# Kernel tuning notes

Measured on AMD Instinct MI355X. Metric: run time of the kernel, lower is better.

The kernel has to match this reference:

```python
import jax, jax.numpy as jnp
import numpy as np

# Model constants (from init_kwargs, post tensor-parallel split with world_size=8)
N_LOCAL_HEADS = 4      # 32 // 8
N_LOCAL_KV_HEADS = 1   # 8 // 8
N_REP = 4              # local q heads per kv head
HEAD_DIM = 128         # 4096 // 32
ROPE_THETA = 500000.0
EPS = 1e-6
FLOOR_SCALE = 8192.0
ATTN_SCALE = 0.1


def setup_inputs() -> dict:
    key = jax.random.key(0)
    ks = jax.random.split(key, 5)
    B, S, D = 4, 2048, 4096
    x = jax.random.normal(ks[0], (B, S, D), dtype=jnp.float32)
    positions = jnp.arange(S, dtype=jnp.int32)
    w_std = 0.02
    wq = jax.random.normal(ks[1], (D, N_LOCAL_HEADS * HEAD_DIM), dtype=jnp.float32) * w_std
    wk = jax.random.normal(ks[2], (D, N_LOCAL_KV_HEADS * HEAD_DIM), dtype=jnp.float32) * w_std
    wv = jax.random.normal(ks[3], (D, N_LOCAL_KV_HEADS * HEAD_DIM), dtype=jnp.float32) * w_std
    wo = jax.random.normal(ks[4], (N_LOCAL_HEADS * HEAD_DIM, D), dtype=jnp.float32) * w_std
    return {"x": x, "positions": positions, "wq": wq, "wk": wk, "wv": wv, "wo": wo}


def _apply_rope(t, cos, sin):
    # t: [B, S, h, HEAD_DIM]; interleaved complex pairs as in torch view_as_complex
    B, S, h, hd = t.shape
    tr = t.reshape(B, S, h, hd // 2, 2)
    t0, t1 = tr[..., 0], tr[..., 1]
    c = cos[None, :, None, :]  # [1, S, 1, hd//2]
    s = sin[None, :, None, :]
    o0 = t0 * c - t1 * s
    o1 = t0 * s + t1 * c
    return jnp.stack([o0, o1], axis=-1).reshape(B, S, h, hd)


def _rms_norm(t):
    # QK-norm: L2/RMS norm over head_dim, no learnable weight (Llama4 style)
    return t * jax.lax.rsqrt(jnp.mean(t * t, axis=-1, keepdims=True) + EPS)


def reference(x, positions, wq, wk, wv, wo):
    B, S, D = x.shape
    q = (x @ wq).reshape(B, S, N_LOCAL_HEADS, HEAD_DIM)
    k = (x @ wk).reshape(B, S, N_LOCAL_KV_HEADS, HEAD_DIM)
    v = (x @ wv).reshape(B, S, N_LOCAL_KV_HEADS, HEAD_DIM)

    # RoPE angles
    pos_f = positions.astype(jnp.float32)
    inv_freq = 1.0 / (ROPE_THETA ** (jnp.arange(0, HEAD_DIM, 2, dtype=jnp.float32) / HEAD_DIM))
    ang = pos_f[:, None] * inv_freq[None, :]  # [S, HEAD_DIM//2]
    cos, sin = jnp.cos(ang), jnp.sin(ang)

    q = _apply_rope(q, cos, sin)
    k = _apply_rope(k, cos, sin)

    # QK RMSNorm (applied after rope)
    q = _rms_norm(q)
    k = _rms_norm(k)

    # Temperature-tuned query scaling (per absolute position)
    attn_scales = jnp.log(jnp.floor((pos_f + 1.0) / FLOOR_SCALE) + 1.0) * ATTN_SCALE + 1.0
    q = q * attn_scales[None, :, None, None]

    # GQA: repeat kv heads to match local query heads
    k = jnp.repeat(k, N_REP, axis=2)  # [B, S, H, hd]
    v = jnp.repeat(v, N_REP, axis=2)

    scale = 1.0 / jnp.sqrt(jnp.float32(HEAD_DIM))
    scores = jnp.einsum("bqhd,bkhd->bhqk", q, k) * scale  # [B, H, S, S]
    causal = jnp.tril(jnp.ones((S, S), dtype=bool))
    scores = jnp.where(causal[None, None, :, :], scores, jnp.finfo(scores.dtype).min)
    probs = jax.nn.softmax(scores, axis=-1)
    attn = jnp.einsum("bhqk,bkhd->bqhd", probs, v).reshape(B, S, N_LOCAL_HEADS * HEAD_DIM)
    return attn @ wo
```

## Files before the change

kernel.cpp:

```cpp
#include <hip/hip_runtime.h>

typedef unsigned short u16;
typedef unsigned int u32;
typedef __bf16 bf16x8 __attribute__((ext_vector_type(8)));
typedef __bf16 bf16x2 __attribute__((ext_vector_type(2)));
typedef float f32x4 __attribute__((ext_vector_type(4)));

#define S_LEN 2048

__device__ __forceinline__ u16 f2b(float f) {
    union { float f; unsigned u; } a; a.f = f;
    unsigned u = a.u;
    unsigned r = u + 0x7fffu + ((u >> 16) & 1u);
    return (u16)(r >> 16);
}

__device__ __forceinline__ u32 pk2(float a, float b) {
    return (u32)f2b(a) | ((u32)f2b(b) << 16);
}

__device__ __forceinline__ u32 cvt2(float lo, float hi) {
    union { bf16x2 v; u32 u; } c;
    c.v[0] = (__bf16)lo; c.v[1] = (__bf16)hi;
    return c.u;
}

__device__ __forceinline__ void gload16(const void* g, void* l) {
    __builtin_amdgcn_global_load_lds(
        (const __attribute__((address_space(1))) unsigned int*)g,
        (__attribute__((address_space(3))) unsigned int*)l,
        16, 0, 0);
}

__global__ __launch_bounds__(256) void pack_wqkv_kernel(const float* __restrict__ wq,
                                                        const float* __restrict__ wk,
                                                        const float* __restrict__ wv,
                                                        u16* __restrict__ W) {
    __shared__ float t[32][33];
    const int n0 = blockIdx.x * 32, k0 = blockIdx.y * 32;
    const int tid = threadIdx.x;
    const int cc = tid & 31, rr = tid >> 5;
    #pragma unroll
    for (int i = 0; i < 4; ++i) {
        int k = k0 + rr + i * 8, n = n0 + cc;
        float v;
        if (n < 512)      v = wq[(size_t)k * 512 + n];
        else if (n < 640) v = wk[(size_t)k * 128 + (n - 512)];
        else              v = wv[(size_t)k * 128 + (n - 640)];
        t[rr + i * 8][cc] = v;
    }
    __syncthreads();
    #pragma unroll
    for (int i = 0; i < 4; ++i) {
        int nn = rr + i * 8, kk = cc;
        W[(size_t)(n0 + nn) * 4096 + k0 + kk] = f2b(t[kk][nn]);
    }
}

__global__ __launch_bounds__(256) void pack_wo_kernel(const float* __restrict__ wo,
                                                      u16* __restrict__ W) {
    __shared__ float t[32][33];
    const int n0 = blockIdx.x * 32, k0 = blockIdx.y * 32;
    const int tid = threadIdx.x;
    const int cc = tid & 31, rr = tid >> 5;
    #pragma unroll
    for (int i = 0; i < 4; ++i)
        t[rr + i * 8][cc] = wo[(size_t)(k0 + rr + i * 8) * 4096 + n0 + cc];
    __syncthreads();
    #pragma unroll
    for (int i = 0; i < 4; ++i)
        W[(size_t)(n0 + rr + i * 8) * 512 + k0 + cc] = f2b(t[cc][rr + i * 8]);
}

__global__ __launch_bounds__(256) void gemm_cvt(const float* __restrict__ A,
                                                const u16* __restrict__ B,
                                                float* __restrict__ C0,
                                                float* __restrict__ C1,
                                                int N, int K, int kBase) {
    __shared__ __align__(16) u16 sB[3][128 * 32];
    __shared__ __align__(16) u16 sAw[4][64 * 40];
    const int tid = threadIdx.x;
    const int lane = tid & 63, wid = tid >> 6;
    const int wr = wid >> 1, wc = wid & 1;
    const int l15 = lane & 15, g = lane >> 4;
    const int srow = lane >> 2;
    const int swzc = ((lane & 3) * 8) ^ (((lane >> 3) & 3) << 3);
    const int rswz = ((l15 >> 1) & 3) << 3;

    const u32 lid = blockIdx.x + gridDim.x * (blockIdx.y + gridDim.y * blockIdx.z);
    const u32 xcd = lid & 7, slot = lid >> 3;
    const u32 per = gridDim.x * gridDim.z;
    const u32 bml = slot / per;
    const u32 rmd = slot - bml * per;
    const int bn = rmd % gridDim.x;
    const int z  = rmd / gridDim.x;
    const int bm = xcd * (gridDim.y >> 3) + bml;

    float* C = z ? C1 : C0;
    const int k0 = z * kBase;
    const int nt = kBase / 32;

    const int ch0 = wid * 2, ch1 = wid * 2 + 1;
    const int br0 = ch0 * 16 + srow, br1 = ch1 * 16 + srow;

    auto stageB = [&](int buf, int kt) {
        gload16(&B[(size_t)(bn * 128 + br0) * K + kt + swzc], &sB[buf][ch0 * 512]);
        gload16(&B[(size_t)(bn * 128 + br1) * K + kt + swzc], &sB[buf][ch1 * 512]);
    };

    const int alr = lane >> 3, alc = (lane & 7) * 4;
    const float* Abase = A + (size_t)(bm * 128 + wr * 64 + alr) * K + alc;

    float4 raw[8];
    auto issueA = [&](int kt) {
        #pragma unroll
        for (int i = 0; i < 8; ++i)
            raw[i] = *(const float4*)(Abase + (size_t)(8 * i) * K + kt);
    };
    auto writeA = [&]() {
        #pragma unroll
        for (int i = 0; i < 8; ++i) {
            uint2 w;
            w.x = cvt2(raw[i].x, raw[i].y);
            w.y = cvt2(raw[i].z, raw[i].w);
            *(uint2*)&sAw[wid][(8 * i + alr) * 40 + alc] = w;
        }
    };

    f32x4 acc[4][4] = {};

    issueA(k0);
    stageB(0, k0);
    stageB(1, k0 + 32);

    for (int t = 0; t < nt; ++t) {
        if (t + 1 < nt) asm volatile("s_waitcnt vmcnt(2)" ::: "memory");
        else            asm volatile("s_waitcnt vmcnt(0)" ::: "memory");
        __builtin_amdgcn_s_barrier();
        writeA();
        if (t + 1 < nt) issueA(k0 + (t + 1) * 32);
        if (t + 2 < nt) stageB((t + 2) % 3, k0 + (t + 2) * 32);
        __builtin_amdgcn_sched_barrier(0);
        const int cur = t % 3;
        bf16x8 af[4], bfr[4];
        #pragma unroll
        for (int m = 0; m < 4; ++m)
            af[m] = *(const bf16x8*)&sAw[wid][(m * 16 + l15) * 40 + g * 8];
        #pragma unroll
        for (int n = 0; n < 4; ++n)
            bfr[n] = *(const bf16x8*)&sB[cur][(wc * 64 + n * 16 + l15) * 32 + (g * 8 ^ rswz)];
        #pragma unroll
        for (int m = 0; m < 4; ++m)
            #pragma unroll
            for (int n = 0; n < 4; ++n)
                acc[m][n] = __builtin_amdgcn_mfma_f32_16x16x32_bf16(af[m], bfr[n], acc[m][n], 0, 0, 0);
    }

    #pragma unroll
    for (int m = 0; m < 4; ++m) {
        int row = bm * 128 + wr * 64 + m * 16 + g * 4;
        #pragma unroll
        for (int n = 0; n < 4; ++n) {
            int col = bn * 128 + wc * 64 + n * 16 + l15;
            #pragma unroll
            for (int rr = 0; rr < 4; ++rr)
                C[(size_t)(row + rr) * N + col] = acc[m][n][rr];
        }
    }
}

__global__ __launch_bounds__(256) void gemm_pipe(const u16* __restrict__ A,
                                                 const u16* __restrict__ B,
                                                 float* __restrict__ C,
                                                 int N, int K) {
    __shared__ __align__(16) u16 sA[3][128 * 32];
    __shared__ __align__(16) u16 sB[3][128 * 32];
    const int tid = threadIdx.x;
    const int lane = tid & 63, wid = tid >> 6;
    const int wr = wid >> 1, wc = wid & 1;
    const int l15 = lane & 15, g = lane >> 4;
    const int srow = lane >> 2;
    const int swzc = ((lane & 3) * 8) ^ (((lane >> 3) & 3) << 3);
    const int rswz = ((l15 >> 1) & 3) << 3;

    const u32 lid = blockIdx.x + gridDim.x * blockIdx.y;
    const u32 xcd = lid & 7, slot = lid >> 3;
    const u32 per = gridDim.x;
    const u32 bml = slot / per;
    const int bn = slot - bml * per;
    const int bm = xcd * (gridDim.y >> 3) + bml;

    const int nt = K / 32;
    const int ch0 = wid * 2, ch1 = wid * 2 + 1;
    const int r0 = ch0 * 16 + srow, r1 = ch1 * 16 + srow;

    auto stage = [&](int buf, int kt) {
        gload16(&A[(size_t)(bm * 128 + r0) * K + kt + swzc], &sA[buf][ch0 * 512]);
        gload16(&A[(size_t)(bm * 128 + r1) * K + kt + swzc], &sA[buf][ch1 * 512]);
        gload16(&B[(size_t)(bn * 128 + r0) * K + kt + swzc], &sB[buf][ch0 * 512]);
        gload16(&B[(size_t)(bn * 128 + r1) * K + kt + swzc], &sB[buf][ch1 * 512]);
    };

    f32x4 acc[4][4] = {};

    stage(0, 0);
    stage(1, 32);

    for (int t = 0; t < nt; ++t) {
        if (t + 1 < nt) asm volatile("s_waitcnt vmcnt(4)" ::: "memory");
        else            asm volatile("s_waitcnt vmcnt(0)" ::: "memory");
        __builtin_amdgcn_s_barrier();
        __builtin_amdgcn_sched_barrier(0);
        if (t + 2 < nt) stage((t + 2) % 3, (t + 2) * 32);
        const int cur = t % 3;
        bf16x8 af[4], bfr[4];
        #pragma unroll
        for (int m = 0; m < 4; ++m)
            af[m] = *(const bf16x8*)&sA[cur][(wr * 64 + m * 16 + l15) * 32 + (g * 8 ^ rswz)];
        #pragma unroll
        for (int n = 0; n < 4; ++n)
            bfr[n] = *(const bf16x8*)&sB[cur][(wc * 64 + n * 16 + l15) * 32 + (g * 8 ^ rswz)];
        #pragma unroll
        for (int m = 0; m < 4; ++m)
            #pragma unroll
            for (int n = 0; n < 4; ++n)
                acc[m][n] = __builtin_amdgcn_mfma_f32_16x16x32_bf16(af[m], bfr[n], acc[m][n], 0, 0, 0);
    }

    #pragma unroll
    for (int m = 0; m < 4; ++m) {
        int row = bm * 128 + wr * 64 + m * 16 + g * 4;
        #pragma unroll
        for (int n = 0; n < 4; ++n) {
            int col = bn * 128 + wc * 64 + n * 16 + l15;
            #pragma unroll
            for (int rr = 0; rr < 4; ++rr)
                C[(size_t)(row + rr) * N + col] = acc[m][n][rr];
        }
    }
}

__global__ __launch_bounds__(256) void rope_rms_kernel(const float* __restrict__ P0,
                                                       const float* __restrict__ P1,
                                                       const int* __restrict__ positions,
                                                       u16* __restrict__ Qb,
                                                       u16* __restrict__ Kb) {
    const int w = blockIdx.x * 4 + (threadIdx.x >> 6);
    const int lane = threadIdx.x & 63;
    const int row = w / 5, head = w - row * 5;
    const int s = row & (S_LEN - 1);

    float pos = (float)positions[s];
    float ex = (float)(2 * lane) * (1.0f / 128.0f);
    float inv_freq = __expf(-ex * 13.122363377404328f);
    float ang = pos * inv_freq;
    float c, sn;
    __sincosf(ang, &sn, &c);

    size_t off = (size_t)row * 768 + head * 128 + 2 * lane;
    float2 va = *(const float2*)&P0[off];
    float2 vb = *(const float2*)&P1[off];
    float x0 = va.x + vb.x, x1 = va.y + vb.y;
    float o0 = x0 * c - x1 * sn;
    float o1 = x0 * sn + x1 * c;

    float ss = o0 * o0 + o1 * o1;
    #pragma unroll
    for (int m = 1; m < 64; m <<= 1) ss += __shfl_xor(ss, m, 64);
    float rms = rsqrtf(ss * (1.0f / 128.0f) + 1e-6f);

    if (head < 4) {
        float ascale = logf(floorf((pos + 1.0f) * (1.0f / 8192.0f)) + 1.0f) * 0.1f + 1.0f;
        float mult = rms * ascale * 0.12751743f;
        *(u32*)&Qb[(size_t)row * 512 + head * 128 + 2 * lane] = pk2(o0 * mult, o1 * mult);
    } else {
        *(u32*)&Kb[(size_t)row * 128 + 2 * lane] = pk2(o0 * rms, o1 * rms);
    }
}

__global__ __launch_bounds__(256) void vtrans_kernel(const float* __restrict__ P0,
                                                     const float* __restrict__ P1,
                                                     u16* __restrict__ Vt) {
    __shared__ u16 tile[128][72];
    const int bi = blockIdx.x >> 5, st = blockIdx.x & 31;
    const int s0 = st * 64;
    const int tid = threadIdx.x;
    #pragma unroll
    for (int i = 0; i < 8; ++i) {
        int idx = i * 256 + tid;
        int r = idx >> 5, c4 = idx & 31;
        size_t off = (size_t)(bi * S_LEN + s0 + r) * 768 + 640 + c4 * 4;
        float4 a = *(const float4*)&P0[off];
        float4 b = *(const float4*)&P1[off];
        tile[c4 * 4 + 0][r] = f2b(a.x + b.x);
        tile[c4 * 4 + 1][r] = f2b(a.y + b.y);
        tile[c4 * 4 + 2][r] = f2b(a.z + b.z);
        tile[c4 * 4 + 3][r] = f2b(a.w + b.w);
    }
    __syncthreads();
    #pragma unroll
    for (int i = 0; i < 4; ++i) {
        int idx = i * 256 + tid;
        int d = idx >> 3, sl = idx & 7;
        bf16x8 v = *(const bf16x8*)&tile[d][sl * 8];
        *(bf16x8*)&Vt[((size_t)bi * 128 + d) * S_LEN + s0 + sl * 8] = v;
    }
}

__global__ __launch_bounds__(256) void attn_kernel(const u16* __restrict__ Qb,
                                                   const u16* __restrict__ Kb,
                                                   const u16* __restrict__ Vt,
                                                   u16* __restrict__ Ob) {
    __shared__ __align__(16) u16 sK[2][64 * 128];
    __shared__ __align__(16) u16 sV[2][128 * 64];
    __shared__ __align__(16) u32 p_all[4][16 * 36];
    const int tid = threadIdx.x;
    const int lane = tid & 63, wid = tid >> 6;
    const int l15 = lane & 15, g = lane >> 4;
    const int bid = blockIdx.x;
    const int qt = 127 - (bid >> 2);
    const int b = bid & 3;
    const int h = wid;
    const int q0 = qt * 16;
    const int kswz = (l15 & 7) << 4;

    u32* p_sh = p_all[wid];

    bf16x8 qf[4];
    {
        const u16* qrow = Qb + (size_t)(b * S_LEN + q0 + l15) * 512 + h * 128 + g * 8;
        #pragma unroll
        for (int c = 0; c < 4; ++c) qf[c] = *(const bf16x8*)(qrow + c * 32);
    }
    const u16* Kbase = Kb + (size_t)b * S_LEN * 128;
    const u16* Vbase = Vt + (size_t)b * 128 * S_LEN;

    const int klr = lane >> 4, klo = (lane & 15) * 16;
    const int vlr = lane >> 3, vlo = (lane & 7) * 16;

    auto stage = [&](int buf, int kv0) {
        #pragma unroll
        for (int j = 0; j < 4; ++j) {
            int r0 = wid * 16 + j * 4;
            int row = r0 + klr;
            gload16((const char*)Kbase + (size_t)(kv0 + row) * 256 + (klo ^ ((row & 7) << 4)),
                    &sK[buf][r0 * 128]);
        }
        #pragma unroll
        for (int j = 0; j < 4; ++j) {
            int r0 = wid * 32 + j * 8;
            int row = r0 + vlr;
            gload16((const char*)Vbase + (size_t)row * (S_LEN * 2) + (size_t)kv0 * 2 + (vlo ^ ((row & 7) << 4)),
                    &sV[buf][r0 * 64]);
        }
    };

    f32x4 oacc[8] = {};
    float m_r = -1e30f, l_r = 0.f;

    const int nt = (q0 >> 6) + 1;
    stage(0, 0);
    __syncthreads();

    for (int t = 0; t < nt; ++t) {
        const u16* sKc = sK[t & 1];
        const u16* sVc = sV[t & 1];
        if (t + 1 < nt) stage((t + 1) & 1, (t + 1) * 64);
        const int kv0 = t * 64;
        const bool masked = (t == nt - 1);

        f32x4 sf[4] = {};
        #pragma unroll
        for (int st = 0; st < 4; ++st) {
            #pragma unroll
            for (int c = 0; c < 4; ++c) {
                bf16x8 kf = *(const bf16x8*)((const char*)sKc +
                                (st * 16 + l15) * 256 + ((c * 64 + g * 16) ^ kswz));
                sf[st] = __builtin_amdgcn_mfma_f32_16x16x32_bf16(kf, qf[c], sf[st], 0, 0, 0);
            }
        }
        float p[16];
        #pragma unroll
        for (int st = 0; st < 4; ++st)
            #pragma unroll
            for (int r = 0; r < 4; ++r) p[st * 4 + r] = sf[st][r];
        if (masked) {
            #pragma unroll
            for (int st = 0; st < 4; ++st)
                #pragma unroll
                for (int r = 0; r < 4; ++r) {
                    int kp = kv0 + st * 16 + g * 4 + r;
                    if (kp > q0 + l15) p[st * 4 + r] = -1e30f;
                }
        }
        float tm = p[0];
        #pragma unroll
        for (int i = 1; i < 16; ++i) tm = fmaxf(tm, p[i]);
        tm = fmaxf(tm, __shfl_xor(tm, 16));
        tm = fmaxf(tm, __shfl_xor(tm, 32));
        float mn = fmaxf(m_r, tm);
        float fscale = exp2f(m_r - mn);
        m_r = mn;
        float rs = 0.f;
        #pragma unroll
        for (int i = 0; i < 16; ++i) { p[i] = exp2f(p[i] - mn); rs += p[i]; }
        rs += __shfl_xor(rs, 16);
        rs += __shfl_xor(rs, 32);
        l_r = l_r * fscale + rs;
        #pragma unroll
        for (int ht = 0; ht < 8; ++ht) oacc[ht] *= fscale;

        #pragma unroll
        for (int st = 0; st < 4; ++st) {
            uint2 w;
            w.x = pk2(p[st * 4 + 0], p[st * 4 + 1]);
            w.y = pk2(p[st * 4 + 2], p[st * 4 + 3]);
            *(uint2*)&p_sh[l15 * 36 + st * 8 + g * 2] = w;
        }
        bf16x8 pa0 = *(const bf16x8*)&p_sh[l15 * 36 + g * 4];
        bf16x8 pa1 = *(const bf16x8*)&p_sh[l15 * 36 + 16 + g * 4];

        #pragma unroll
        for (int ht = 0; ht < 8; ++ht) {
            bf16x8 v0 = *(const bf16x8*)((const char*)sVc +
                            (ht * 16 + l15) * 128 + ((g * 16) ^ kswz));
            bf16x8 v1 = *(const bf16x8*)((const char*)sVc +
                            (ht * 16 + l15) * 128 + ((64 + g * 16) ^ kswz));
            oacc[ht] = __builtin_amdgcn_mfma_f32_16x16x32_bf16(v0, pa0, oacc[ht], 0, 0, 0);
            oacc[ht] = __builtin_amdgcn_mfma_f32_16x16x32_bf16(v1, pa1, oacc[ht], 0, 0, 0);
        }
        __syncthreads();
    }

    float inv_l = 1.0f / l_r;
    #pragma unroll
    for (int ht = 0; ht < 8; ++ht) {
        uint2 o;
        o.x = pk2(oacc[ht][0] * inv_l, oacc[ht][1] * inv_l);
        o.y = pk2(oacc[ht][2] * inv_l, oacc[ht][3] * inv_l);
        *(uint2*)&Ob[(size_t)(b * S_LEN + q0 + l15) * 512 + h * 128 + ht * 16 + g * 4] = o;
    }
}

extern "C" void kernel_launch(void* const* d_in, const int* in_sizes, int n_in,
                              void* d_out, int out_size, void* d_ws, size_t ws_size,
                              hipStream_t stream) {
    const float* x         = (const float*)d_in[0];
    const int*   positions = (const int*)d_in[1];
    const float* wq        = (const float*)d_in[2];
    const float* wk        = (const float*)d_in[3];
    const float* wv        = (const float*)d_in[4];
    const float* wo        = (const float*)d_in[5];
    float* out = (float*)d_out;

    float* P1 = (float*)((char*)d_out + 67108864);

    char* ws = (char*)d_ws;
    size_t off = 0;
    auto alloc = [&](size_t bytes) { void* p = ws + off; off = (off + bytes + 255) & ~(size_t)255; return p; };
    u16*   Wqkv = (u16*)alloc(768ull * 4096 * 2);
    u16*   WoT  = (u16*)alloc(4096ull * 512 * 2);
    float* P0   = (float*)alloc(8192ull * 768 * 4);
    u16*   Qb   = (u16*)alloc(8192ull * 512 * 2);
    u16*   Kb   = (u16*)alloc(8192ull * 128 * 2);
    u16*   Vt   = (u16*)alloc(4ull * 128 * 2048 * 2);
    u16*   Ob   = (u16*)alloc(8192ull * 512 * 2);

    pack_wqkv_kernel<<<dim3(24, 128), 256, 0, stream>>>(wq, wk, wv, Wqkv);
    pack_wo_kernel<<<dim3(128, 16), 256, 0, stream>>>(wo, WoT);

    gemm_cvt<<<dim3(6, 64, 2), 256, 0, stream>>>(x, Wqkv, P0, P1, 768, 4096, 2048);

    rope_rms_kernel<<<(8192 * 5) / 4, 256, 0, stream>>>(P0, P1, positions, Qb, Kb);
    vtrans_kernel<<<128, 256, 0, stream>>>(P0, P1, Vt);

    attn_kernel<<<512, 256, 0, stream>>>(Qb, Kb, Vt, Ob);

    gemm_pipe<<<dim3(32, 64), 256, 0, stream>>>(Ob, WoT, out, 4096, 512);
}
```

Baseline: 267.0 us.

## Pre-convert x to bf16 and use async LDS-load GEMM with bf16 split-K partials

Adds a standalone kernel that converts x to bf16 into the output buffer, then replaces the fp32-A converting GEMM with one that streams both operands via global_load_lds into a triple-buffered pipeline. The split-K partial outputs are now stored as bf16 instead of fp32, and the rope and V-transpose kernels read and sum bf16 partials. This removes the per-thread register staging and conversion from the GEMM main loop and halves partial traffic. In exchange it adds an extra full pass over x (read fp32, write bf16) and loses precision on the partial sums.

```diff
diff --git a/kernel.cpp b/kernel.cpp
--- a/kernel.cpp
+++ b/kernel.cpp
@@ -3,7 +3,6 @@
 typedef unsigned short u16;
 typedef unsigned int u32;
 typedef __bf16 bf16x8 __attribute__((ext_vector_type(8)));
-typedef __bf16 bf16x2 __attribute__((ext_vector_type(2)));
 typedef float f32x4 __attribute__((ext_vector_type(4)));
 
 #define S_LEN 2048
@@ -15,14 +14,12 @@
     return (u16)(r >> 16);
 }
 
+__device__ __forceinline__ float b2f(u32 h) {
+    union { u32 u; float f; } c; c.u = h << 16; return c.f;
+}
+
 __device__ __forceinline__ u32 pk2(float a, float b) {
     return (u32)f2b(a) | ((u32)f2b(b) << 16);
-}
-
-__device__ __forceinline__ u32 cvt2(float lo, float hi) {
-    union { bf16x2 v; u32 u; } c;
-    c.v[0] = (__bf16)lo; c.v[1] = (__bf16)hi;
-    return c.u;
 }
 
 __device__ __forceinline__ void gload16(const void* g, void* l) {
@@ -30,6 +27,15 @@
         (const __attribute__((address_space(1))) unsigned int*)g,
         (__attribute__((address_space(3))) unsigned int*)l,
         16, 0, 0);
+}
+
+__global__ __launch_bounds__(256) void conv_x_kernel(const float* __restrict__ x,
+                                                     u16* __restrict__ xb) {
+    long i = ((long)blockIdx.x * 256 + threadIdx.x) * 4;
+    float4 v = *(const float4*)(x + i);
+    ushort4 o;
+    o.x = f2b(v.x); o.y = f2b(v.y); o.z = f2b(v.z); o.w = f2b(v.w);
+    *(ushort4*)(xb + i) = o;
 }
 
 __global__ __launch_bounds__(256) void pack_wqkv_kernel(const float* __restrict__ wq,
@@ -72,13 +78,13 @@
         W[(size_t)(n0 + rr + i * 8) * 512 + k0 + cc] = f2b(t[cc][rr + i * 8]);
 }
 
-__global__ __launch_bounds__(256) void gemm_cvt(const float* __restrict__ A,
-                                                const u16* __restrict__ B,
-                                                float* __restrict__ C0,
-                                                float* __restrict__ C1,
-                                                int N, int K, int kBase) {
+__global__ __launch_bounds__(256) void gemm_pipe_bf(const u16* __restrict__ A,
+                                                    const u16* __restrict__ B,
+                                                    u16* __restrict__ C0,
+                                                    u16* __restrict__ C1,
+                                                    int N, int K, int kBase) {
+    __shared__ __align__(16) u16 sA[3][128 * 32];
     __shared__ __align__(16) u16 sB[3][128 * 32];
-    __shared__ __align__(16) u16 sAw[4][64 * 40];
     const int tid = threadIdx.x;
     const int lane = tid & 63, wid = tid >> 6;
     const int wr = wid >> 1, wc = wid & 1;
@@ -96,56 +102,36 @@
     const int z  = rmd / gridDim.x;
     const int bm = xcd * (gridDim.y >> 3) + bml;
 
-    float* C = z ? C1 : C0;
+    u16* C = z ? C1 : C0;
     const int k0 = z * kBase;
     const int nt = kBase / 32;
 
     const int ch0 = wid * 2, ch1 = wid * 2 + 1;
-    const int br0 = ch0 * 16 + srow, br1 = ch1 * 16 + srow;
-
-    auto stageB = [&](int buf, int kt) {
-        gload16(&B[(size_t)(bn * 128 + br0) * K + kt + swzc], &sB[buf][ch0 * 512]);
-        gload16(&B[(size_t)(bn * 128 + br1) * K + kt + swzc], &sB[buf][ch1 * 512]);
+    const int r0 = ch0 * 16 + srow, r1 = ch1 * 16 + srow;
+
+    auto stage = [&](int buf, int kt) {
+        gload16(&A[(size_t)(bm * 128 + r0) * K + kt + swzc], &sA[buf][ch0 * 512]);
+        gload16(&A[(size_t)(bm * 128 + r1) * K + kt + swzc], &sA[buf][ch1 * 512]);
+        gload16(&B[(size_t)(bn * 128 + r0) * K + kt + swzc], &sB[buf][ch0 * 512]);
+        gload16(&B[(size_t)(bn * 128 + r1) * K + kt + swzc], &sB[buf][ch1 * 512]);
     };
 
-    const int alr = lane >> 3, alc = (lane & 7) * 4;
-    const float* Abase = A + (size_t)(bm * 128 + wr * 64 + alr) * K + alc;
-
-    float4 raw[8];
-    auto issueA = [&](int kt) {
-        #pragma unroll
-        for (int i = 0; i < 8; ++i)
-            raw[i] = *(const float4*)(Abase + (size_t)(8 * i) * K + kt);
-    };
-    auto writeA = [&]() {
-        #pragma unroll
-        for (int i = 0; i < 8; ++i) {
-            uint2 w;
-            w.x = cvt2(raw[i].x, raw[i].y);
-            w.y = cvt2(raw[i].z, raw[i].w);
-            *(uint2*)&sAw[wid][(8 * i + alr) * 40 + alc] = w;
-        }
-    };
-
     f32x4 acc[4][4] = {};
 
-    issueA(k0);
-    stageB(0, k0);
-    stageB(1, k0 + 32);
+    stage(0, k0);
+    stage(1, k0 + 32);
 
     for (int t = 0; t < nt; ++t) {
-        if (t + 1 < nt) asm volatile("s_waitcnt vmcnt(2)" ::: "memory");
+        if (t + 1 < nt) asm volatile("s_waitcnt vmcnt(4)" ::: "memory");
         else            asm volatile("s_waitcnt vmcnt(0)" ::: "memory");
         __builtin_amdgcn_s_barrier();
-        writeA();
-        if (t + 1 < nt) issueA(k0 + (t + 1) * 32);
-        if (t + 2 < nt) stageB((t + 2) % 3, k0 + (t + 2) * 32);
         __builtin_amdgcn_sched_barrier(0);
+        if (t + 2 < nt) stage((t + 2) % 3, k0 + (t + 2) * 32);
         const int cur = t % 3;
         bf16x8 af[4], bfr[4];
         #pragma unroll
         for (int m = 0; m < 4; ++m)
-            af[m] = *(const bf16x8*)&sAw[wid][(m * 16 + l15) * 40 + g * 8];
+            af[m] = *(const bf16x8*)&sA[cur][(wr * 64 + m * 16 + l15) * 32 + (g * 8 ^ rswz)];
         #pragma unroll
         for (int n = 0; n < 4; ++n)
             bfr[n] = *(const bf16x8*)&sB[cur][(wc * 64 + n * 16 + l15) * 32 + (g * 8 ^ rswz)];
@@ -164,7 +150,7 @@
             int col = bn * 128 + wc * 64 + n * 16 + l15;
             #pragma unroll
             for (int rr = 0; rr < 4; ++rr)
-                C[(size_t)(row + rr) * N + col] = acc[m][n][rr];
+                C[(size_t)(row + rr) * N + col] = f2b(acc[m][n][rr]);
         }
     }
 }
@@ -240,8 +226,8 @@
     }
 }
 
-__global__ __launch_bounds__(256) void rope_rms_kernel(const float* __restrict__ P0,
-                                                       const float* __restrict__ P1,
+__global__ __launch_bounds__(256) void rope_rms_kernel(const u16* __restrict__ P0,
+                                                       const u16* __restrict__ P1,
                                                        const int* __restrict__ positions,
                                                        u16* __restrict__ Qb,
                                                        u16* __restrict__ Kb) {
@@ -258,9 +244,10 @@
     __sincosf(ang, &sn, &c);
 
     size_t off = (size_t)row * 768 + head * 128 + 2 * lane;
-    float2 va = *(const float2*)&P0[off];
-    float2 vb = *(const float2*)&P1[off];
-    float x0 = va.x + vb.x, x1 = va.y + vb.y;
+    u32 pa = *(const u32*)&P0[off];
+    u32 pb = *(const u32*)&P1[off];
+    float x0 = b2f(pa & 0xffffu) + b2f(pb & 0xffffu);
+    float x1 = b2f(pa >> 16)     + b2f(pb >> 16);
     float o0 = x0 * c - x1 * sn;
     float o1 = x0 * sn + x1 * c;
 
@@ -278,8 +265,8 @@
     }
 }
 
-__global__ __launch_bounds__(256) void vtrans_kernel(const float* __restrict__ P0,
-                                                     const float* __restrict__ P1,
+__global__ __launch_bounds__(256) void vtrans_kernel(const u16* __restrict__ P0,
+                                                     const u16* __restrict__ P1,
                                                      u16* __restrict__ Vt) {
     __shared__ u16 tile[128][72];
     const int bi = blockIdx.x >> 5, st = blockIdx.x & 31;
@@ -290,12 +277,12 @@
         int idx = i * 256 + tid;
         int r = idx >> 5, c4 = idx & 31;
         size_t off = (size_t)(bi * S_LEN + s0 + r) * 768 + 640 + c4 * 4;
-        float4 a = *(const float4*)&P0[off];
-        float4 b = *(const float4*)&P1[off];
-        tile[c4 * 4 + 0][r] = f2b(a.x + b.x);
-        tile[c4 * 4 + 1][r] = f2b(a.y + b.y);
-        tile[c4 * 4 + 2][r] = f2b(a.z + b.z);
-        tile[c4 * 4 + 3][r] = f2b(a.w + b.w);
+        uint2 a = *(const uint2*)&P0[off];
+        uint2 b = *(const uint2*)&P1[off];
+        tile[c4 * 4 + 0][r] = f2b(b2f(a.x & 0xffffu) + b2f(b.x & 0xffffu));
+        tile[c4 * 4 + 1][r] = f2b(b2f(a.x >> 16)     + b2f(b.x >> 16));
+        tile[c4 * 4 + 2][r] = f2b(b2f(a.y & 0xffffu) + b2f(b.y & 0xffffu));
+        tile[c4 * 4 + 3][r] = f2b(b2f(a.y >> 16)     + b2f(b.y >> 16));
     }
     __syncthreads();
     #pragma unroll
@@ -453,23 +440,25 @@
     const float* wo        = (const float*)d_in[5];
     float* out = (float*)d_out;
 
-    float* P1 = (float*)((char*)d_out + 67108864);
+    u16* Xb = (u16*)d_out;
+    u16* P1 = (u16*)((char*)d_out + 67108864);
 
     char* ws = (char*)d_ws;
     size_t off = 0;
     auto alloc = [&](size_t bytes) { void* p = ws + off; off = (off + bytes + 255) & ~(size_t)255; return p; };
     u16*   Wqkv = (u16*)alloc(768ull * 4096 * 2);
     u16*   WoT  = (u16*)alloc(4096ull * 512 * 2);
-    float* P0   = (float*)alloc(8192ull * 768 * 4);
+    u16*   P0   = (u16*)alloc(8192ull * 768 * 2);
     u16*   Qb   = (u16*)alloc(8192ull * 512 * 2);
     u16*   Kb   = (u16*)alloc(8192ull * 128 * 2);
     u16*   Vt   = (u16*)alloc(4ull * 128 * 2048 * 2);
     u16*   Ob   = (u16*)alloc(8192ull * 512 * 2);
 
+    conv_x_kernel<<<(8192 * 4096) / (4 * 256), 256, 0, stream>>>(x, Xb);
     pack_wqkv_kernel<<<dim3(24, 128), 256, 0, stream>>>(wq, wk, wv, Wqkv);
     pack_wo_kernel<<<dim3(128, 16), 256, 0, stream>>>(wo, WoT);
 
-    gemm_cvt<<<dim3(6, 64, 2), 256, 0, stream>>>(x, Wqkv, P0, P1, 768, 4096, 2048);
+    gemm_pipe_bf<<<dim3(6, 64, 2), 256, 0, stream>>>(Xb, Wqkv, P0, P1, 768, 4096, 2048);
 
     rope_rms_kernel<<<(8192 * 5) / 4, 256, 0, stream>>>(P0, P1, positions, Qb, Kb);
     vtrans_kernel<<<128, 256, 0, stream>>>(P0, P1, Vt);
```

New measurement: 243.1 us. -9.0%, faster.
